# Kernel optimization log

Hardware: AMD Instinct MI355X
Metric: run time of the kernel (lower is better)

Reference implementation:

```python
import jax, jax.numpy as jnp
import numpy as np

B, N, D, K = 8, 2048, 512, 16  # batch, points, feature dim, similar_num
EPS = 1e-8


def setup_inputs() -> dict:
    key = jax.random.key(0)
    ks = jax.random.split(key, 9)
    p = jax.random.normal(ks[0], (B, N, 3), dtype=jnp.float32)
    q = jax.random.normal(ks[1], (B, N, 3), dtype=jnp.float32)
    ffp = jax.random.normal(ks[2], (B, N, D), dtype=jnp.float32)
    ffq = jax.random.normal(ks[3], (B, N, D), dtype=jnp.float32)
    eye = jnp.eye(3, dtype=jnp.float32)
    # near-identity perturbed rotations so inverse is well-conditioned
    R1 = eye + 0.1 * jax.random.normal(ks[4], (B, N, 3, 3), dtype=jnp.float32)
    R2 = eye + 0.1 * jax.random.normal(ks[5], (B, N, 3, 3), dtype=jnp.float32)
    centroids = jax.random.randint(ks[6], (B, N), 0, 2 * N)  # FPS indices into 2N pts
    W = 0.02 * jax.random.normal(ks[7], (3, 3 * D), dtype=jnp.float32)  # refine_net pointwise linear
    b = jnp.zeros((3,), dtype=jnp.float32)
    return {"p": p, "q": q, "ffp": ffp, "ffq": ffq, "R1": R1, "R2": R2,
            "centroids": centroids, "W": W, "b": b}


def _forward(p, q, ffp, ffq, R1, R2, centroids, W, b):
    # cosine similarity between query features (ffq) and source features (ffp): [B,N,N]
    fq = ffq / (jnp.linalg.norm(ffq, axis=-1, keepdims=True) + EPS)
    fp = ffp / (jnp.linalg.norm(ffp, axis=-1, keepdims=True) + EPS)
    w1 = jnp.einsum('bqd,bpd->bqp', fq, fp)
    _, idx = jax.lax.top_k(w1, K)                      # [B,N,K] neighbor indices into ffp
    feat = jax.vmap(lambda z, i: z[i])(ffp, idx)       # batched gather -> [B,N,K,D]
    # adaptive_{avg,max}_pool2d over the K axis, then cat(avg, max): [B,N,2D]
    f_agg = jnp.concatenate([feat.mean(axis=2), feat.max(axis=2)], axis=-1)
    f1 = jnp.concatenate([ffq, f_agg], axis=-1)        # [B,N,3D]
    vec = jnp.einsum('bnd,od->bno', f1, W) + b         # refine_net -> [B,N,3]
    vec = jnp.linalg.inv(R1) @ vec[..., None]          # rotate back (R1^-1)
    vec = (jnp.linalg.inv(R2) @ vec)[..., 0]           # rotate back (R2^-1) -> [B,N,3]
    mask = (centroids >= p.shape[1]).astype(vec.dtype)[..., None]
    q_refine = q + vec * mask
    return q_refine, idx


def reference(p, q, ffp, ffq, R1, R2, centroids, W, b):
    q_refine, similar_idx = _forward(p, q, ffp, ffq, R1, R2, centroids, W, b)
    # original returns (q_cat, q_refine, q_refine, similar_idx)
    return (q, q_refine, q_refine, similar_idx)
```

## Files before the change

kernel.cpp:

```cpp
#include <hip/hip_runtime.h>
#include <math.h>

#define BB 8
#define NN 2048
#define DD 512
#define KK 16
#define BN (BB*NN)

#define QT 64
#define JSPLIT 4
#define JRANGE (NN/JSPLIT)
#define MM (16*JSPLIT)
#define SIMP 68

#define KSPLIT 384

#define OUT1 (BN*3)
#define OUT2 (2*BN*3)
#define OUT3 (3*BN*3)

typedef __attribute__((ext_vector_type(8))) short bf16x8;
typedef __attribute__((ext_vector_type(4))) float f32x4;

__device__ inline unsigned short cvt_bf16(float f) {
    unsigned int u = __float_as_uint(f);
    return (unsigned short)((u + 0x7fffu + ((u >> 16) & 1u)) >> 16);
}

__device__ inline void gload_lds16(const unsigned short* g, unsigned short* lds) {
    __builtin_amdgcn_global_load_lds((const __attribute__((address_space(1))) void*)g,
                                     (__attribute__((address_space(3))) void*)lds,
                                     16, 0, 0);
}

__global__ __launch_bounds__(256) void k_norm_np(const float* __restrict__ ffq,
                                                 const float* __restrict__ ffp,
                                                 float* __restrict__ normq,
                                                 float* __restrict__ normp,
                                                 float* __restrict__ rnp32) {
    const int row = blockIdx.x * 32 + (threadIdx.x >> 3);
    const int j   = threadIdx.x & 7;
    const bool isQ = row < BN;
    const int r = isQ ? row : row - BN;
    const float* x = (isQ ? ffq : ffp) + (size_t)r * DD;

    float B[4];
#pragma unroll
    for (int t = 0; t < 4; ++t) {
        const float* xb = x + t * 128;
        float e = xb[j];
        float rj = __fmul_rn(e, e);
#pragma unroll
        for (int i = 1; i < 16; ++i) {
            float v = xb[8 * i + j];
            rj = __fadd_rn(rj, __fmul_rn(v, v));
        }
        float s = __fadd_rn(rj, __shfl_xor(rj, 1, 8));
        float u = __fadd_rn(s,  __shfl_xor(s,  2, 8));
        float w = __fadd_rn(u,  __shfl_xor(u,  4, 8));
        B[t] = w;
    }
    if (j == 0) {
        float norm2 = __fadd_rn(__fadd_rn(B[0], B[1]), __fadd_rn(B[2], B[3]));
        float nrm = __fsqrt_rn(norm2);
        if (isQ) { normq[r] = nrm; }
        else {
            normp[r] = nrm;
            rnp32[r] = 1.0f / __fadd_rn(nrm, 1e-8f);
        }
    }
}

__global__ __launch_bounds__(256) void k_normalize(const float* __restrict__ ffq,
                                                   const float* __restrict__ ffp,
                                                   const float* __restrict__ normq,
                                                   const float* __restrict__ normp,
                                                   float* __restrict__ fqn,
                                                   float* __restrict__ fpn,
                                                   unsigned short* __restrict__ fqb,
                                                   unsigned short* __restrict__ fpb) {
    const size_t e4 = ((size_t)blockIdx.x * 256 + threadIdx.x) * 4;
    if (e4 >= (size_t)BN * DD) return;
    const int row = (int)(e4 >> 9);
    {
        float4 v = *(const float4*)(ffq + e4);
        float den = __fadd_rn(normq[row], 1e-8f);
        float4 o;
        o.x = __fdiv_rn(v.x, den); o.y = __fdiv_rn(v.y, den);
        o.z = __fdiv_rn(v.z, den); o.w = __fdiv_rn(v.w, den);
        *(float4*)(fqn + e4) = o;
        ushort4 b; b.x = cvt_bf16(o.x); b.y = cvt_bf16(o.y);
        b.z = cvt_bf16(o.z); b.w = cvt_bf16(o.w);
        *(ushort4*)(fqb + e4) = b;
    }
    {
        float4 v = *(const float4*)(ffp + e4);
        float den = __fadd_rn(normp[row], 1e-8f);
        float4 o;
        o.x = __fdiv_rn(v.x, den); o.y = __fdiv_rn(v.y, den);
        o.z = __fdiv_rn(v.z, den); o.w = __fdiv_rn(v.w, den);
        *(float4*)(fpn + e4) = o;
        ushort4 b; b.x = cvt_bf16(o.x); b.y = cvt_bf16(o.y);
        b.z = cvt_bf16(o.z); b.w = cvt_bf16(o.w);
        *(ushort4*)(fpb + e4) = b;
    }
}

#define CK 128
__global__ __launch_bounds__(256)
__attribute__((amdgpu_waves_per_eu(2, 4)))
void k_phase1_m(const unsigned short* __restrict__ fqb,
                const unsigned short* __restrict__ fpb,
                unsigned short* __restrict__ cand) {
    __shared__ __align__(16) float simb[QT * SIMP];
    __shared__ __align__(16) unsigned short Bst[64 * CK];

    const int b  = blockIdx.x & 7;
    const int i0 = ((blockIdx.x >> 3) & 31) * QT;
    const int js = blockIdx.x >> 8;
    const int tid = threadIdx.x;
    const int w = tid >> 6, lane = tid & 63;
    const int n16 = lane & 15, quad = lane >> 4;

    const unsigned short* Aq = fqb + ((size_t)b * NN + i0 + w * 16 + n16) * DD + quad * 8;
    bf16x8 afr[16];
#pragma unroll
    for (int kt = 0; kt < 16; ++kt)
        afr[kt] = *(const bf16x8*)(Aq + kt * 32);

    float tv[16]; int tix[16];
#pragma unroll
    for (int r = 0; r < 16; ++r) { tv[r] = -INFINITY; tix[r] = -1; }

    const int qq = tid >> 2;
    const int st = tid & 3;
    const size_t bNN = (size_t)b * NN;

    for (int jt = 0; jt < JRANGE / 64; ++jt) {
        const int j0g = js * JRANGE + jt * 64;

        f32x4 acc[4];
#pragma unroll
        for (int ct = 0; ct < 4; ++ct) acc[ct] = (f32x4){0.f, 0.f, 0.f, 0.f};

        for (int kc = 0; kc < 4; ++kc) {
            __syncthreads();
#pragma unroll
            for (int l = 0; l < 4; ++l) {
                const int r  = (w * 4 + l) * 4 + quad;
                const int sb = n16 ^ (r & 15);
                const unsigned short* gsrc =
                    fpb + (bNN + j0g + r) * DD + kc * CK + sb * 8;
                gload_lds16(gsrc, &Bst[(w * 4 + l) * 512]);
            }
            __syncthreads();
#pragma unroll
            for (int k4 = 0; k4 < 4; ++k4) {
#pragma unroll
                for (int ct = 0; ct < 4; ++ct) {
                    const int r  = ct * 16 + n16;
                    const int cb = (k4 * 4 + quad) ^ (r & 15);
                    bf16x8 bfr = *(const bf16x8*)&Bst[r * CK + cb * 8];
                    acc[ct] = __builtin_amdgcn_mfma_f32_16x16x32_bf16(
                        afr[kc * 4 + k4], bfr, acc[ct], 0, 0, 0);
                }
            }
        }

        __syncthreads();
#pragma unroll
        for (int ct = 0; ct < 4; ++ct)
#pragma unroll
            for (int r = 0; r < 4; ++r)
                simb[(w * 16 + quad * 4 + r) * SIMP + ct * 16 + n16] = acc[ct][r];
        __syncthreads();

#pragma unroll
        for (int t4 = 0; t4 < 4; ++t4) {
            const float4 v4 = *(const float4*)&simb[qq * SIMP + st * 16 + t4 * 4];
            const float vm = fmaxf(fmaxf(v4.x, v4.y), fmaxf(v4.z, v4.w));
            if (vm > tv[0]) {
                const float vv[4] = {v4.x, v4.y, v4.z, v4.w};
#pragma unroll
                for (int u = 0; u < 4; ++u) {
                    const float v = vv[u];
                    const int jg = j0g + st * 16 + t4 * 4 + u;
                    if (v > tv[0]) {
#pragma unroll
                        for (int r = 0; r < 15; ++r) {
                            const bool up = tv[r + 1] < v;
                            const float nv = up ? tv[r + 1] : ((tv[r] < v) ? v : tv[r]);
                            const int   ni = up ? tix[r + 1] : ((tv[r] < v) ? jg : tix[r]);
                            tv[r] = nv; tix[r] = ni;
                        }
                        if (tv[15] < v) { tv[15] = v; tix[15] = jg; }
                    }
                }
            }
        }
    }

    __syncthreads();
    int p = 15;
    const size_t base = ((size_t)b * NN + i0 + qq) * MM + (size_t)js * 16;
    for (int m = 0; m < 16; ++m) {
        float cv = (p >= 0) ? tv[p] : -INFINITY;
        int   ci = (p >= 0) ? tix[p] : -1;
        float ov; int oi;
        ov = __shfl_xor(cv, 1, 4); oi = __shfl_xor(ci, 1, 4);
        if (ov > cv || (ov == cv && (unsigned)oi < (unsigned)ci)) { cv = ov; ci = oi; }
        ov = __shfl_xor(cv, 2, 4); oi = __shfl_xor(ci, 2, 4);
        if (ov > cv || (ov == cv && (unsigned)oi < (unsigned)ci)) { cv = ov; ci = oi; }
        if (p >= 0 && tv[p] == cv && tix[p] == ci) --p;
        if (st == 0) cand[base + m] = (unsigned short)ci;
    }
}

#define JTILE 64
#define BK 16
#define LDP 68
__global__ __launch_bounds__(256, 4) void k_phase1_v(const float* __restrict__ ffq,
                                                     const float* __restrict__ ffp,
                                                     const float* __restrict__ rnp32,
                                                     unsigned short* __restrict__ cand) {
    __shared__ __align__(16) float As[BK * LDP];
    __shared__ __align__(16) float Bs[BK * LDP];
    __shared__ __align__(16) float simb[QT * SIMP];

    const int b  = blockIdx.x & 7;
    const int i0 = ((blockIdx.x >> 3) & 31) * QT;
    const int js = blockIdx.x >> 8;
    const int tid = threadIdx.x;
    const int tx = tid & 15, ty = tid >> 4;

    const float* Abase = ffq + ((size_t)b * NN + i0) * DD;
    const float* Bbase = ffp + (size_t)b * NN * DD;

    float tv[16]; int tix[16];
#pragma unroll
    for (int r = 0; r < 16; ++r) { tv[r] = -INFINITY; tix[r] = -1; }

    const int lrow = tid >> 2;
    const int lseg = (tid & 3) * 4;
    const int qq = tid >> 2;
    const int st = tid & 3;

    for (int jt = 0; jt < JRANGE / JTILE; ++jt) {
        const int j0 = js * JRANGE + jt * JTILE;
        float acc[4][4];
#pragma unroll
        for (int r = 0; r < 4; ++r)
#pragma unroll
            for (int c = 0; c < 4; ++c) acc[r][c] = 0.0f;

        for (int kt = 0; kt < DD / BK; ++kt) {
            const int k0 = kt * BK;
            __syncthreads();
            float4 av = *(const float4*)(Abase + (size_t)lrow * DD + k0 + lseg);
            float4 bv = *(const float4*)(Bbase + (size_t)(j0 + lrow) * DD + k0 + lseg);
            As[(lseg + 0) * LDP + lrow] = av.x; As[(lseg + 1) * LDP + lrow] = av.y;
            As[(lseg + 2) * LDP + lrow] = av.z; As[(lseg + 3) * LDP + lrow] = av.w;
            Bs[(lseg + 0) * LDP + lrow] = bv.x; Bs[(lseg + 1) * LDP + lrow] = bv.y;
            Bs[(lseg + 2) * LDP + lrow] = bv.z; Bs[(lseg + 3) * LDP + lrow] = bv.w;
            __syncthreads();
#pragma unroll
            for (int kk = 0; kk < BK; ++kk) {
                const float4 a4 = *(const float4*)&As[kk * LDP + ty * 4];
                const float4 b4 = *(const float4*)&Bs[kk * LDP + tx * 4];
                const float ar[4] = {a4.x, a4.y, a4.z, a4.w};
                const float br[4] = {b4.x, b4.y, b4.z, b4.w};
#pragma unroll
                for (int r = 0; r < 4; ++r)
#pragma unroll
                    for (int c = 0; c < 4; ++c)
                        acc[r][c] = fmaf(ar[r], br[c], acc[r][c]);
            }
        }
        float rp[4];
#pragma unroll
        for (int c = 0; c < 4; ++c) rp[c] = rnp32[b * NN + j0 + tx * 4 + c];
#pragma unroll
        for (int r = 0; r < 4; ++r) {
            float4 v4;
            v4.x = acc[r][0] * rp[0]; v4.y = acc[r][1] * rp[1];
            v4.z = acc[r][2] * rp[2]; v4.w = acc[r][3] * rp[3];
            *(float4*)&simb[(ty * 4 + r) * SIMP + tx * 4] = v4;
        }
        __syncthreads();

#pragma unroll
        for (int t = 0; t < 16; ++t) {
            const int jl = st * 16 + t;
            const float v = simb[qq * SIMP + jl];
            const int jg = j0 + jl;
            if (v > tv[0]) {
#pragma unroll
                for (int r = 0; r < 15; ++r) {
                    const bool up = tv[r + 1] < v;
                    const float nv = up ? tv[r + 1] : ((tv[r] < v) ? v : tv[r]);
                    const int   ni = up ? tix[r + 1] : ((tv[r] < v) ? jg : tix[r]);
                    tv[r] = nv; tix[r] = ni;
                }
                if (tv[15] < v) { tv[15] = v; tix[15] = jg; }
            }
        }
        __syncthreads();
    }

    int p = 15;
    const size_t base = ((size_t)b * NN + i0 + qq) * MM + (size_t)js * 16;
    for (int m = 0; m < 16; ++m) {
        float cv = (p >= 0) ? tv[p] : -INFINITY;
        int   ci = (p >= 0) ? tix[p] : -1;
        float ov; int oi;
        ov = __shfl_xor(cv, 1, 4); oi = __shfl_xor(ci, 1, 4);
        if (ov > cv || (ov == cv && (unsigned)oi < (unsigned)ci)) { cv = ov; ci = oi; }
        ov = __shfl_xor(cv, 2, 4); oi = __shfl_xor(ci, 2, 4);
        if (ov > cv || (ov == cv && (unsigned)oi < (unsigned)ci)) { cv = ov; ci = oi; }
        if (p >= 0 && tv[p] == cv && tix[p] == ci) --p;
        if (st == 0) cand[base + m] = (unsigned short)ci;
    }
}

__device__ inline void inv3_apply(const double* a, double x0, double x1, double x2,
                                  double& y0, double& y1, double& y2) {
    double c00 = a[4]*a[8] - a[5]*a[7];
    double c01 = a[2]*a[7] - a[1]*a[8];
    double c02 = a[1]*a[5] - a[2]*a[4];
    double c10 = a[5]*a[6] - a[3]*a[8];
    double c11 = a[0]*a[8] - a[2]*a[6];
    double c12 = a[2]*a[3] - a[0]*a[5];
    double c20 = a[3]*a[7] - a[4]*a[6];
    double c21 = a[1]*a[6] - a[0]*a[7];
    double c22 = a[0]*a[4] - a[1]*a[3];
    double det = a[0]*c00 + a[1]*c10 + a[2]*c20;
    double id = 1.0 / det;
    y0 = (c00*x0 + c01*x1 + c02*x2) * id;
    y1 = (c10*x0 + c11*x1 + c12*x2) * id;
    y2 = (c20*x0 + c21*x1 + c22*x2) * id;
}

#define STG_S 65
template <bool PRE>
__device__ inline void phase2_body(
        const float* __restrict__ qin, const float* __restrict__ ffq,
        const float* __restrict__ ffp, const float* __restrict__ R1,
        const float* __restrict__ R2, const int* __restrict__ cent,
        const float* __restrict__ W, const float* __restrict__ bvec,
        const float* __restrict__ normq, const float* __restrict__ normp,
        const float* __restrict__ fqn, const float* __restrict__ fpn,
        const unsigned short* __restrict__ cand, float* __restrict__ out) {
    static_assert(KSPLIT == 384, "chunk split at c=6 assumes KSPLIT==384");
    const int b = blockIdx.x & 7;
    const int i = blockIdx.x >> 3;
    const int tid = threadIdx.x;
    const size_t qi = (size_t)b * NN + i;

    __shared__ float sfqn[DD];
    __shared__ int cj[MM];
    __shared__ float pden_s[MM];
    __shared__ float sv[MM];
    __shared__ int sel[KK];
    __shared__ __align__(16) float stg[MM * STG_S];
    __shared__ float red[3][4];
    float* const meanf = stg;
    float* const maxf  = stg + DD;

    if (PRE) {
        for (int d = tid; d < DD; d += 256)
            sfqn[d] = fqn[qi * DD + d];
    } else {
        const float qden = __fadd_rn(normq[qi], 1e-8f);
        for (int d = tid; d < DD; d += 256)
            sfqn[d] = __fdiv_rn(ffq[qi * DD + d], qden);
    }
    if (tid < MM) {
        int j = (int)cand[qi * MM + tid];
        cj[tid] = j;
        if (!PRE) pden_s[tid] = __fadd_rn(normp[(size_t)b * NN + j], 1e-8f);
    }
    __syncthreads();

    const int srow = tid >> 2;
    const int slan = tid & 3;
    const float* fprow = (PRE ? fpn : ffp) + ((size_t)b * NN + cj[srow]) * DD;
    const float pd = (!PRE) ? pden_s[tid < MM ? tid : 0] : 1.0f;
    float acc1 = 0.0f, acc2 = 0.0f;

    auto stg_write = [&](const float4* P) {
#pragma unroll
        for (int i4 = 0; i4 < 4; ++i4) {
            const int off = srow * STG_S + i4 * 16 + slan * 4;
            stg[off + 0] = P[i4].x; stg[off + 1] = P[i4].y;
            stg[off + 2] = P[i4].z; stg[off + 3] = P[i4].w;
        }
    };
    auto ld_chunk = [&](float4* P, int c) {
#pragma unroll
        for (int i4 = 0; i4 < 4; ++i4)
            P[i4] = *(const float4*)(fprow + c * 64 + i4 * 16 + slan * 4);
    };
    auto chain = [&](int c, float& acc) {
        const int d0 = c * 64;
        const float* s = stg + tid * STG_S;
        if (PRE) {
#pragma unroll
            for (int k = 0; k < 64; ++k)
                acc = fmaf(sfqn[d0 + k], s[k], acc);
        } else {
#pragma unroll
            for (int k = 0; k < 64; ++k)
                acc = fmaf(sfqn[d0 + k], __fdiv_rn(s[k], pd), acc);
        }
    };

    float4 pA[4], pB[4];
    ld_chunk(pA, 0);
#pragma unroll
    for (int ch = 0; ch < 4; ++ch) {
        {
            const int c0 = 2 * ch;
            stg_write(pA);
            ld_chunk(pB, c0 + 1);
            __syncthreads();
            if (tid < MM) chain(c0, (c0 < 6) ? acc1 : acc2);
            __syncthreads();
        }
        {
            const int c1 = 2 * ch + 1;
            stg_write(pB);
            if (ch < 3) ld_chunk(pA, c1 + 1);
            __syncthreads();
            if (tid < MM) chain(c1, (c1 < 6) ? acc1 : acc2);
            __syncthreads();
        }
    }
    if (tid < MM) sv[tid] = __fadd_rn(acc1, acc2);
    __syncthreads();

    if (tid < MM) {
        const float v = sv[tid]; const int jj = cj[tid];
        int rank = 0;
        for (int t = 0; t < MM; ++t) {
            const float vt = sv[t]; const int jo = cj[t];
            rank += (vt > v) || (vt == v && jo < jj);
        }
        if (rank < KK) {
            sel[rank] = jj;
            out[(size_t)OUT3 + qi * KK + rank] = (float)jj;
        }
    }
    __syncthreads();

    for (int d = tid; d < DD; d += 256) {
        float sum = 0.0f, mx = -INFINITY;
#pragma unroll
        for (int k = 0; k < KK; ++k) {
            float v = ffp[((size_t)b * NN + sel[k]) * DD + d];
            sum += v; mx = fmaxf(mx, v);
        }
        meanf[d] = sum * (1.0f / 16.0f);
        maxf[d]  = mx;
    }
    __syncthreads();

    float a0 = 0.f, a1 = 0.f, a2 = 0.f;
    for (int d = tid; d < DD; d += 256) {
        const float x = ffq[qi * DD + d], m = meanf[d], mx = maxf[d];
        a0 = fmaf(W[d],        x, a0); a0 = fmaf(W[512 + d],        m, a0); a0 = fmaf(W[1024 + d],        mx, a0);
        a1 = fmaf(W[1536 + d], x, a1); a1 = fmaf(W[1536 + 512 + d], m, a1); a1 = fmaf(W[1536 + 1024 + d], mx, a1);
        a2 = fmaf(W[3072 + d], x, a2); a2 = fmaf(W[3072 + 512 + d], m, a2); a2 = fmaf(W[3072 + 1024 + d], mx, a2);
    }
#pragma unroll
    for (int off = 32; off > 0; off >>= 1) {
        a0 += __shfl_down(a0, off, 64);
        a1 += __shfl_down(a1, off, 64);
        a2 += __shfl_down(a2, off, 64);
    }
    const int lane = tid & 63, wid = tid >> 6;
    if (lane == 0) { red[0][wid] = a0; red[1][wid] = a1; red[2][wid] = a2; }
    __syncthreads();

    if (tid == 0) {
        double v0 = (double)bvec[0] + red[0][0] + red[0][1] + red[0][2] + red[0][3];
        double v1 = (double)bvec[1] + red[1][0] + red[1][1] + red[1][2] + red[1][3];
        double v2 = (double)bvec[2] + red[2][0] + red[2][1] + red[2][2] + red[2][3];
        double r1[9], r2[9];
#pragma unroll
        for (int t = 0; t < 9; ++t) { r1[t] = R1[qi * 9 + t]; r2[t] = R2[qi * 9 + t]; }
        double u0, u1, u2, w0, w1, w2;
        inv3_apply(r1, v0, v1, v2, u0, u1, u2);
        inv3_apply(r2, u0, u1, u2, w0, w1, w2);
        const float mask = (cent[qi] >= NN) ? 1.0f : 0.0f;
        const float q0 = qin[qi * 3 + 0], q1 = qin[qi * 3 + 1], q2 = qin[qi * 3 + 2];
        out[qi * 3 + 0] = q0; out[qi * 3 + 1] = q1; out[qi * 3 + 2] = q2;
        const float o0 = q0 + (float)w0 * mask;
        const float o1 = q1 + (float)w1 * mask;
        const float o2 = q2 + (float)w2 * mask;
        out[OUT1 + qi * 3 + 0] = o0; out[OUT1 + qi * 3 + 1] = o1; out[OUT1 + qi * 3 + 2] = o2;
        out[OUT2 + qi * 3 + 0] = o0; out[OUT2 + qi * 3 + 1] = o1; out[OUT2 + qi * 3 + 2] = o2;
    }
}

__global__ __launch_bounds__(256, 8) void k_phase2_f(
        const float* qin, const float* ffq, const float* ffp, const float* R1,
        const float* R2, const int* cent, const float* W, const float* bvec,
        const float* fqn, const float* fpn, const unsigned short* cand, float* out) {
    phase2_body<true>(qin, ffq, ffp, R1, R2, cent, W, bvec,
                      nullptr, nullptr, fqn, fpn, cand, out);
}

__global__ __launch_bounds__(256, 8) void k_phase2_v(
        const float* qin, const float* ffq, const float* ffp, const float* R1,
        const float* R2, const int* cent, const float* W, const float* bvec,
        const float* normq, const float* normp, const unsigned short* cand, float* out) {
    phase2_body<false>(qin, ffq, ffp, R1, R2, cent, W, bvec,
                       normq, normp, nullptr, nullptr, cand, out);
}

extern "C" void kernel_launch(void* const* d_in, const int* in_sizes, int n_in,
                              void* d_out, int out_size, void* d_ws, size_t ws_size,
                              hipStream_t stream) {
    (void)in_sizes; (void)n_in; (void)out_size;
    const float* q   = (const float*)d_in[1];
    const float* ffp = (const float*)d_in[2];
    const float* ffq = (const float*)d_in[3];
    const float* R1  = (const float*)d_in[4];
    const float* R2  = (const float*)d_in[5];
    const int*   ct  = (const int*)d_in[6];
    const float* W   = (const float*)d_in[7];
    const float* bb  = (const float*)d_in[8];
    float* out = (float*)d_out;

    float* normq = (float*)d_ws;
    float* normp = normq + BN;
    float* rnp32 = normp + BN;
    unsigned short* cand = (unsigned short*)(rnp32 + BN);
    float* fqn = (float*)(cand + (size_t)BN * MM);
    float* fpn = fqn + (size_t)BN * DD;
    unsigned short* fqb = (unsigned short*)(fpn + (size_t)BN * DD);
    unsigned short* fpb = fqb + (size_t)BN * DD;

    const size_t need = (size_t)BN * (35 * 4 + 2 * DD * 4 + 2 * DD * 2);

    k_norm_np<<<dim3((2 * BN) / 32), dim3(256), 0, stream>>>(ffq, ffp, normq, normp, rnp32);

    if (ws_size >= need) {
        k_normalize<<<dim3((BN * DD) / 1024), dim3(256), 0, stream>>>(
            ffq, ffp, normq, normp, fqn, fpn, fqb, fpb);
        k_phase1_m<<<dim3(BB * (NN / QT) * JSPLIT), dim3(256), 0, stream>>>(fqb, fpb, cand);
        k_phase2_f<<<dim3(BB * NN), dim3(256), 0, stream>>>(q, ffq, ffp, R1, R2, ct, W, bb,
                                                            fqn, fpn, cand, out);
    } else {
        k_phase1_v<<<dim3(BB * (NN / QT) * JSPLIT), dim3(256), 0, stream>>>(ffq, ffp, rnp32, cand);
        k_phase2_v<<<dim3(BB * NN), dim3(256), 0, stream>>>(q, ffq, ffp, R1, R2, ct, W, bb,
                                                            normq, normp, cand, out);
    }
}
```

Baseline: 512.7 us.

## Double-buffer B tile staging with async global-to-LDS prefetch in phase1

```diff
diff --git a/kernel.cpp b/kernel.cpp
--- a/kernel.cpp
+++ b/kernel.cpp
@@ -32,6 +32,9 @@
                                      (__attribute__((address_space(3))) void*)lds,
                                      16, 0, 0);
 }
+
+__device__ inline void waitcnt_vm4() { asm volatile("s_waitcnt vmcnt(4)" ::: "memory"); }
+__device__ inline void waitcnt_vm0() { asm volatile("s_waitcnt vmcnt(0)" ::: "memory"); }
 
 __global__ __launch_bounds__(256) void k_norm_np(const float* __restrict__ ffq,
                                                  const float* __restrict__ ffp,
@@ -113,7 +116,7 @@
                 const unsigned short* __restrict__ fpb,
                 unsigned short* __restrict__ cand) {
     __shared__ __align__(16) float simb[QT * SIMP];
-    __shared__ __align__(16) unsigned short Bst[64 * CK];
+    __shared__ __align__(16) unsigned short Bst[2 * 64 * CK];
 
     const int b  = blockIdx.x & 7;
     const int i0 = ((blockIdx.x >> 3) & 31) * QT;
@@ -136,43 +139,59 @@
     const int st = tid & 3;
     const size_t bNN = (size_t)b * NN;
 
-    for (int jt = 0; jt < JRANGE / 64; ++jt) {
+    auto stage_chunk = [&](int jt, int kc, unsigned short* dst) {
         const int j0g = js * JRANGE + jt * 64;
-
-        f32x4 acc[4];
-#pragma unroll
-        for (int ct = 0; ct < 4; ++ct) acc[ct] = (f32x4){0.f, 0.f, 0.f, 0.f};
-
+#pragma unroll
+        for (int l = 0; l < 4; ++l) {
+            const int r  = (w * 4 + l) * 4 + quad;
+            const int sb = n16 ^ (r & 15);
+            const unsigned short* gsrc =
+                fpb + (bNN + j0g + r) * DD + kc * CK + sb * 8;
+            gload_lds16(gsrc, dst + (w * 4 + l) * 512);
+        }
+    };
+
+    f32x4 acc[4];
+#pragma unroll
+    for (int ct = 0; ct < 4; ++ct) acc[ct] = (f32x4){0.f, 0.f, 0.f, 0.f};
+
+    stage_chunk(0, 0, &Bst[0]);
+
+    for (int jt = 0; jt < 8; ++jt) {
+#pragma unroll
         for (int kc = 0; kc < 4; ++kc) {
-            __syncthreads();
-#pragma unroll
-            for (int l = 0; l < 4; ++l) {
-                const int r  = (w * 4 + l) * 4 + quad;
-                const int sb = n16 ^ (r & 15);
-                const unsigned short* gsrc =
-                    fpb + (bNN + j0g + r) * DD + kc * CK + sb * 8;
-                gload_lds16(gsrc, &Bst[(w * 4 + l) * 512]);
+            const bool haveNext = (jt < 7) || (kc < 3);
+            if (haveNext) {
+                const int njt = (kc == 3) ? jt + 1 : jt;
+                const int nkc = (kc + 1) & 3;
+                stage_chunk(njt, nkc, &Bst[((kc + 1) & 1) * 8192]);
             }
-            __syncthreads();
+            if (haveNext) waitcnt_vm4(); else waitcnt_vm0();
+            __builtin_amdgcn_s_barrier();
+            __builtin_amdgcn_sched_barrier(0);
+            const unsigned short* bcur = &Bst[(kc & 1) * 8192];
 #pragma unroll
             for (int k4 = 0; k4 < 4; ++k4) {
 #pragma unroll
                 for (int ct = 0; ct < 4; ++ct) {
                     const int r  = ct * 16 + n16;
                     const int cb = (k4 * 4 + quad) ^ (r & 15);
-                    bf16x8 bfr = *(const bf16x8*)&Bst[r * CK + cb * 8];
+                    bf16x8 bfr = *(const bf16x8*)&bcur[r * CK + cb * 8];
                     acc[ct] = __builtin_amdgcn_mfma_f32_16x16x32_bf16(
                         afr[kc * 4 + k4], bfr, acc[ct], 0, 0, 0);
                 }
             }
-        }
-
-        __syncthreads();
-#pragma unroll
-        for (int ct = 0; ct < 4; ++ct)
+            __builtin_amdgcn_s_barrier();
+        }
+
+        const int j0g = js * JRANGE + jt * 64;
+#pragma unroll
+        for (int ct = 0; ct < 4; ++ct) {
 #pragma unroll
             for (int r = 0; r < 4; ++r)
                 simb[(w * 16 + quad * 4 + r) * SIMP + ct * 16 + n16] = acc[ct][r];
+            acc[ct] = (f32x4){0.f, 0.f, 0.f, 0.f};
+        }
         __syncthreads();
 
 #pragma unroll
```

Result: faster. 501.8 us (-2.1%).
